# Performance work log

Measured on AMD Instinct MI355X. Metric: run time of the kernel, lower is better.

Reference implementation:

```python
import jax, jax.numpy as jnp
import numpy as np

H = 512  # hidden_size


def setup_inputs() -> dict:
    key = jax.random.key(0)
    k1, k2, k3, k4, k5, k6 = jax.random.split(key, 6)
    B, S = 32, 2048
    output = jax.random.normal(k1, (B, H), dtype=jnp.float32)
    encoder_outputs = jax.random.normal(k2, (B, S, 2 * H), dtype=jnp.float32)
    encoder_mask = jax.random.randint(k3, (B, S), 0, 2, dtype=jnp.int32)
    # nn.Linear(3H, H): weight [H, 3H], bias [H]
    bound = 1.0 / np.sqrt(3 * H)
    W_attn = jax.random.uniform(k4, (H, 3 * H), minval=-bound, maxval=bound, dtype=jnp.float32)
    b_attn = jax.random.uniform(k5, (H,), minval=-bound, maxval=bound, dtype=jnp.float32)
    v = jax.random.normal(k6, (H,), dtype=jnp.float32) * (1.0 / np.sqrt(H))
    return {"output": output, "encoder_outputs": encoder_outputs,
            "encoder_mask": encoder_mask, "W_attn": W_attn, "b_attn": b_attn, "v": v}


def reference(output, encoder_outputs, encoder_mask, W_attn, b_attn, v):
    # Equivalent to cat([repeat(output), enc], -1) @ W.T: split W into state/enc blocks
    W_s = W_attn[:, :H]        # [H, H]   acts on decoder state
    W_e = W_attn[:, H:]        # [H, 2H]  acts on encoder outputs
    state_proj = output @ W_s.T                              # [B, H]
    enc_proj = jnp.einsum('bse,he->bsh', encoder_outputs, W_e)  # [B, S, H]
    energy = jnp.tanh(state_proj[:, None, :] + enc_proj + b_attn)  # [B, S, H]
    scores = jnp.einsum('bsh,h->bs', energy, v)[:, None, :]   # [B, 1, S]
    scores = scores - 1000.0 * (encoder_mask[:, None, :] == 0).astype(scores.dtype)
    return jax.nn.softmax(scores, axis=2)
```

## Files before the change

### kernel.cpp

```cpp
#include <hip/hip_runtime.h>
#include <hip/hip_bf16.h>

typedef __attribute__((ext_vector_type(4))) float f32x4;
typedef __attribute__((ext_vector_type(8))) short short8;

#define HH 512
#define BB 32
#define SS 2048
#define KK 1024

__device__ __forceinline__ unsigned short f2bf(float f) {
    unsigned int u = __float_as_uint(f);
    u += 0x7fffu + ((u >> 16) & 1u);
    return (unsigned short)(u >> 16);
}

__device__ __forceinline__ float fast_tanh(float x) {
    float e = __expf(2.0f * x);
    return 1.0f - 2.0f / (e + 1.0f);
}

__global__ __launch_bounds__(256)
void spb_kernel(const float* __restrict__ out_state,
                const float* __restrict__ W,
                const float* __restrict__ bias,
                float* __restrict__ spb) {
    int wave = threadIdx.x >> 6, lane = threadIdx.x & 63;
    int g = blockIdx.x * 4 + wave;
    int b = g >> 9, h = g & 511;
    const float* wr = W + (size_t)h * 1536;
    const float* ov = out_state + b * HH;
    float4 w0 = *(const float4*)(wr + lane * 8);
    float4 w1 = *(const float4*)(wr + lane * 8 + 4);
    float4 o0 = *(const float4*)(ov + lane * 8);
    float4 o1 = *(const float4*)(ov + lane * 8 + 4);
    float d = w0.x * o0.x + w0.y * o0.y + w0.z * o0.z + w0.w * o0.w
            + w1.x * o1.x + w1.y * o1.y + w1.z * o1.z + w1.w * o1.w;
    d += __shfl_xor(d, 1); d += __shfl_xor(d, 2); d += __shfl_xor(d, 4);
    d += __shfl_xor(d, 8); d += __shfl_xor(d, 16); d += __shfl_xor(d, 32);
    if (lane == 0) spb[g] = d + bias[h];
}

__global__ void wconv_kernel(const float* __restrict__ W, unsigned short* __restrict__ Wt) {
    int idx = blockIdx.x * 256 + threadIdx.x;
    int e8 = idx * 8;
    int h = e8 >> 10;
    int k = e8 & 1023;
    const float* src = W + (size_t)h * 1536 + 512 + k;
    float4 w0 = *(const float4*)src;
    float4 w1 = *(const float4*)(src + 4);
    int kt = k >> 5;
    int q  = (k >> 3) & 3;
    int g  = h >> 4;
    int r  = h & 15;
    int ln = (q << 4) | r;
    unsigned short* dst = Wt + (size_t)kt * 16384 + g * 512 + ln * 8;
    ushort4 p0, p1;
    p0.x = f2bf(w0.x); p0.y = f2bf(w0.y); p0.z = f2bf(w0.z); p0.w = f2bf(w0.w);
    p1.x = f2bf(w1.x); p1.y = f2bf(w1.y); p1.z = f2bf(w1.z); p1.w = f2bf(w1.w);
    *(ushort4*)dst = p0;
    *(ushort4*)(dst + 4) = p1;
}

__global__ __launch_bounds__(512, 4)
void attn_gemm(const float* __restrict__ enc, const unsigned short* __restrict__ Wt,
               const float* __restrict__ spb, const float* __restrict__ vvec,
               float* __restrict__ scores) {
    __shared__ unsigned short Asm[2 * 64 * 32];
    __shared__ float red[8][64];

    const int tid = threadIdx.x;
    const int w = tid >> 6;
    const int lane = tid & 63;
    const int r = lane & 15;
    const int q = lane >> 4;
    const int b = blockIdx.x >> 5;
    const int s0 = (blockIdx.x & 31) << 6;

    const int arow = tid >> 3;
    const int akq = tid & 7;
    const float4* aptr = (const float4*)(enc + ((size_t)(b * SS + s0 + arow)) * KK + akq * 4);
    const int st_off = arow * 32 + akq * 4;
    const int rd_off = r * 32 + q * 8;
    const unsigned short* wbase = Wt + (size_t)w * 2048 + lane * 8;

    f32x4 acc[4][4] = {};

    float4 f = aptr[0]; aptr += 8;
    {
        ushort4 p;
        p.x = f2bf(f.x); p.y = f2bf(f.y); p.z = f2bf(f.z); p.w = f2bf(f.w);
        *(ushort4*)(Asm + st_off) = p;
    }
    __syncthreads();

    for (int kt = 0; kt < 31; ++kt) {
        float4 fn = aptr[0]; aptr += 8;

        const short8* wp = (const short8*)(wbase + (size_t)kt * 16384);
        short8 bf[4];
        #pragma unroll
        for (int nf = 0; nf < 4; ++nf) bf[nf] = wp[nf * 64];

        const short8* ap = (const short8*)(Asm + (kt & 1) * 2048 + rd_off);
        short8 af[4];
        #pragma unroll
        for (int mt = 0; mt < 4; ++mt) af[mt] = ap[mt * 64];

        #pragma unroll
        for (int mt = 0; mt < 4; ++mt)
            #pragma unroll
            for (int nf = 0; nf < 4; ++nf)
                acc[mt][nf] = __builtin_amdgcn_mfma_f32_16x16x32_bf16(
                    af[mt], bf[nf], acc[mt][nf], 0, 0, 0);

        ushort4 p;
        p.x = f2bf(fn.x); p.y = f2bf(fn.y); p.z = f2bf(fn.z); p.w = f2bf(fn.w);
        *(ushort4*)(Asm + ((kt + 1) & 1) * 2048 + st_off) = p;
        __syncthreads();
    }
    {
        const short8* wp = (const short8*)(wbase + (size_t)31 * 16384);
        short8 bf[4];
        #pragma unroll
        for (int nf = 0; nf < 4; ++nf) bf[nf] = wp[nf * 64];
        const short8* ap = (const short8*)(Asm + (31 & 1) * 2048 + rd_off);
        short8 af[4];
        #pragma unroll
        for (int mt = 0; mt < 4; ++mt) af[mt] = ap[mt * 64];
        #pragma unroll
        for (int mt = 0; mt < 4; ++mt)
            #pragma unroll
            for (int nf = 0; nf < 4; ++nf)
                acc[mt][nf] = __builtin_amdgcn_mfma_f32_16x16x32_bf16(
                    af[mt], bf[nf], acc[mt][nf], 0, 0, 0);
    }

    float vh[4], sh[4];
    #pragma unroll
    for (int nf = 0; nf < 4; ++nf) {
        int h = w * 64 + nf * 16 + r;
        vh[nf] = vvec[h];
        sh[nf] = spb[b * HH + h];
    }
    float rowacc[4][4] = {};
    #pragma unroll
    for (int mt = 0; mt < 4; ++mt)
        #pragma unroll
        for (int nf = 0; nf < 4; ++nf)
            #pragma unroll
            for (int i = 0; i < 4; ++i) {
                float x = acc[mt][nf][i] + sh[nf];
                rowacc[mt][i] += vh[nf] * fast_tanh(x);
            }
    #pragma unroll
    for (int mt = 0; mt < 4; ++mt)
        #pragma unroll
        for (int i = 0; i < 4; ++i) {
            float t = rowacc[mt][i];
            t += __shfl_xor(t, 1);
            t += __shfl_xor(t, 2);
            t += __shfl_xor(t, 4);
            t += __shfl_xor(t, 8);
            rowacc[mt][i] = t;
        }
    if (r == 0) {
        #pragma unroll
        for (int mt = 0; mt < 4; ++mt)
            #pragma unroll
            for (int i = 0; i < 4; ++i)
                red[w][mt * 16 + q * 4 + i] = rowacc[mt][i];
    }
    __syncthreads();
    if (tid < 64) {
        float sum = 0.f;
        #pragma unroll
        for (int ww = 0; ww < 8; ++ww) sum += red[ww][tid];
        scores[b * SS + s0 + tid] = sum;
    }
}

__global__ void softmax_kernel(const float* __restrict__ scores,
                               const int* __restrict__ mask,
                               float* __restrict__ out) {
    __shared__ float red[256];
    int b = blockIdx.x, tid = threadIdx.x;
    float x[8];
    #pragma unroll
    for (int i = 0; i < 8; ++i) {
        int s = tid + i * 256;
        float sc = scores[b * SS + s];
        if (mask[b * SS + s] == 0) sc -= 1000.0f;
        x[i] = sc;
    }
    float mx = x[0];
    #pragma unroll
    for (int i = 1; i < 8; ++i) mx = fmaxf(mx, x[i]);
    red[tid] = mx;
    __syncthreads();
    for (int o = 128; o > 0; o >>= 1) {
        if (tid < o) red[tid] = fmaxf(red[tid], red[tid + o]);
        __syncthreads();
    }
    mx = red[0];
    __syncthreads();
    float e[8], sum = 0.f;
    #pragma unroll
    for (int i = 0; i < 8; ++i) { e[i] = __expf(x[i] - mx); sum += e[i]; }
    red[tid] = sum;
    __syncthreads();
    for (int o = 128; o > 0; o >>= 1) {
        if (tid < o) red[tid] += red[tid + o];
        __syncthreads();
    }
    float inv = 1.0f / red[0];
    #pragma unroll
    for (int i = 0; i < 8; ++i) out[b * SS + tid + i * 256] = e[i] * inv;
}

extern "C" void kernel_launch(void* const* d_in, const int* in_sizes, int n_in,
                              void* d_out, int out_size, void* d_ws, size_t ws_size,
                              hipStream_t stream) {
    const float* out_state = (const float*)d_in[0];
    const float* enc       = (const float*)d_in[1];
    const int*   mask      = (const int*)d_in[2];
    const float* W_attn    = (const float*)d_in[3];
    const float* b_attn    = (const float*)d_in[4];
    const float* vvec      = (const float*)d_in[5];
    float* out = (float*)d_out;

    char* ws = (char*)d_ws;
    float*          spb    = (float*)ws;
    unsigned short* Wt     = (unsigned short*)(ws + 65536);
    float*          scores = (float*)(ws + 65536 + 1048576);

    spb_kernel<<<4096, 256, 0, stream>>>(out_state, W_attn, b_attn, spb);
    wconv_kernel<<<256, 256, 0, stream>>>(W_attn, Wt);
    attn_gemm<<<1024, 512, 0, stream>>>(enc, Wt, spb, vvec, scores);
    softmax_kernel<<<32, 256, 0, stream>>>(scores, mask, out);
}
```

Baseline: 437.4 us.

## Stage four K-tiles per barrier in attention GEMM to deepen prefetch

The encoder-tile pipeline now loads four 32-wide K slices per thread (128 columns) per stage into a larger double-buffered LDS area, computes four MFMA sub-steps, then syncs once. This cuts the barriers from 32 to 8 and puts more global loads in flight to hide latency. In exchange it raises LDS use from 8KB to 32KB per block and adds registers for the prefetched float4s, which may reduce occupancy.

New measurement: 429.1 us. Within noise of the previous version (-1.9%).

```diff
diff --git a/kernel.cpp b/kernel.cpp
--- a/kernel.cpp
+++ b/kernel.cpp
@@ -13,6 +13,12 @@
     unsigned int u = __float_as_uint(f);
     u += 0x7fffu + ((u >> 16) & 1u);
     return (unsigned short)(u >> 16);
+}
+
+__device__ __forceinline__ ushort4 pack4(float4 f) {
+    ushort4 p;
+    p.x = f2bf(f.x); p.y = f2bf(f.y); p.z = f2bf(f.z); p.w = f2bf(f.w);
+    return p;
 }
 
 __device__ __forceinline__ float fast_tanh(float x) {
@@ -55,18 +61,15 @@
     int r  = h & 15;
     int ln = (q << 4) | r;
     unsigned short* dst = Wt + (size_t)kt * 16384 + g * 512 + ln * 8;
-    ushort4 p0, p1;
-    p0.x = f2bf(w0.x); p0.y = f2bf(w0.y); p0.z = f2bf(w0.z); p0.w = f2bf(w0.w);
-    p1.x = f2bf(w1.x); p1.y = f2bf(w1.y); p1.z = f2bf(w1.z); p1.w = f2bf(w1.w);
-    *(ushort4*)dst = p0;
-    *(ushort4*)(dst + 4) = p1;
+    *(ushort4*)dst = pack4(w0);
+    *(ushort4*)(dst + 4) = pack4(w1);
 }
 
 __global__ __launch_bounds__(512, 4)
 void attn_gemm(const float* __restrict__ enc, const unsigned short* __restrict__ Wt,
                const float* __restrict__ spb, const float* __restrict__ vvec,
                float* __restrict__ scores) {
-    __shared__ unsigned short Asm[2 * 64 * 32];
+    __shared__ unsigned short Asm[2 * 8192];
     __shared__ float red[8][64];
 
     const int tid = threadIdx.x;
@@ -79,61 +82,53 @@
 
     const int arow = tid >> 3;
     const int akq = tid & 7;
-    const float4* aptr = (const float4*)(enc + ((size_t)(b * SS + s0 + arow)) * KK + akq * 4);
-    const int st_off = arow * 32 + akq * 4;
+    const float* arowp = enc + ((size_t)(b * SS + s0 + arow)) * KK + akq * 4;
+    const int st_off = tid * 4;
     const int rd_off = r * 32 + q * 8;
     const unsigned short* wbase = Wt + (size_t)w * 2048 + lane * 8;
 
     f32x4 acc[4][4] = {};
-
-    float4 f = aptr[0]; aptr += 8;
-    {
-        ushort4 p;
-        p.x = f2bf(f.x); p.y = f2bf(f.y); p.z = f2bf(f.z); p.w = f2bf(f.w);
-        *(ushort4*)(Asm + st_off) = p;
-    }
-    __syncthreads();
-
-    for (int kt = 0; kt < 31; ++kt) {
-        float4 fn = aptr[0]; aptr += 8;
-
-        const short8* wp = (const short8*)(wbase + (size_t)kt * 16384);
-        short8 bf[4];
-        #pragma unroll
-        for (int nf = 0; nf < 4; ++nf) bf[nf] = wp[nf * 64];
-
-        const short8* ap = (const short8*)(Asm + (kt & 1) * 2048 + rd_off);
-        short8 af[4];
-        #pragma unroll
-        for (int mt = 0; mt < 4; ++mt) af[mt] = ap[mt * 64];
-
-        #pragma unroll
-        for (int mt = 0; mt < 4; ++mt)
-            #pragma unroll
-            for (int nf = 0; nf < 4; ++nf)
-                acc[mt][nf] = __builtin_amdgcn_mfma_f32_16x16x32_bf16(
-                    af[mt], bf[nf], acc[mt][nf], 0, 0, 0);
-
-        ushort4 p;
-        p.x = f2bf(fn.x); p.y = f2bf(fn.y); p.z = f2bf(fn.z); p.w = f2bf(fn.w);
-        *(ushort4*)(Asm + ((kt + 1) & 1) * 2048 + st_off) = p;
-        __syncthreads();
-    }
-    {
-        const short8* wp = (const short8*)(wbase + (size_t)31 * 16384);
-        short8 bf[4];
-        #pragma unroll
-        for (int nf = 0; nf < 4; ++nf) bf[nf] = wp[nf * 64];
-        const short8* ap = (const short8*)(Asm + (31 & 1) * 2048 + rd_off);
-        short8 af[4];
-        #pragma unroll
-        for (int mt = 0; mt < 4; ++mt) af[mt] = ap[mt * 64];
-        #pragma unroll
-        for (int mt = 0; mt < 4; ++mt)
-            #pragma unroll
-            for (int nf = 0; nf < 4; ++nf)
-                acc[mt][nf] = __builtin_amdgcn_mfma_f32_16x16x32_bf16(
-                    af[mt], bf[nf], acc[mt][nf], 0, 0, 0);
+    float4 f[4];
+
+    #pragma unroll
+    for (int t = 0; t < 4; ++t) f[t] = *(const float4*)(arowp + t * 32);
+    #pragma unroll
+    for (int t = 0; t < 4; ++t)
+        *(ushort4*)(Asm + t * 2048 + st_off) = pack4(f[t]);
+    __syncthreads();
+
+    for (int p = 0; p < 8; ++p) {
+        const int buf = p & 1;
+        if (p < 7) {
+            const float* src = arowp + (p + 1) * 128;
+            #pragma unroll
+            for (int t = 0; t < 4; ++t) f[t] = *(const float4*)(src + t * 32);
+        }
+        #pragma unroll
+        for (int sub = 0; sub < 4; ++sub) {
+            const int kt = p * 4 + sub;
+            const short8* wp = (const short8*)(wbase + (size_t)kt * 16384);
+            short8 bf[4];
+            #pragma unroll
+            for (int nf = 0; nf < 4; ++nf) bf[nf] = wp[nf * 64];
+            const short8* ap = (const short8*)(Asm + buf * 8192 + sub * 2048 + rd_off);
+            short8 af[4];
+            #pragma unroll
+            for (int mt = 0; mt < 4; ++mt) af[mt] = ap[mt * 64];
+            #pragma unroll
+            for (int mt = 0; mt < 4; ++mt)
+                #pragma unroll
+                for (int nf = 0; nf < 4; ++nf)
+                    acc[mt][nf] = __builtin_amdgcn_mfma_f32_16x16x32_bf16(
+                        af[mt], bf[nf], acc[mt][nf], 0, 0, 0);
+        }
+        if (p < 7) {
+            unsigned short* dst = Asm + (buf ^ 1) * 8192 + st_off;
+            #pragma unroll
+            for (int t = 0; t < 4; ++t)
+                *(ushort4*)(dst + t * 2048) = pack4(f[t]);
+            __syncthreads();
+        }
     }
 
     float vh[4], sh[4];
```
